# Kernel tuning notes

Measured on AMD Instinct MI355X. Metric: run time of the kernel, lower is better.

The kernel has to match this reference:

```python
import jax, jax.numpy as jnp
import numpy as np

NEG_SLOPE = 0.2

def gat_conv(x, src, dst, W, a_src, a_dst, bias, num_nodes, heads, out_ch, concat):
    # x: [N, Fin]; W: [Fin, heads*out_ch]; a_src/a_dst: [heads, out_ch]
    h = (x @ W).reshape(num_nodes, heads, out_ch)            # [N,H,C]
    alpha_s = jnp.einsum('nhc,hc->nh', h, a_src)             # [N,H]
    alpha_d = jnp.einsum('nhc,hc->nh', h, a_dst)             # [N,H]
    e = alpha_s[src] + alpha_d[dst]                          # [E,H]
    e = jnp.where(e > 0, e, NEG_SLOPE * e)                   # LeakyReLU
    # segment softmax over incoming edges per destination node
    m = jax.ops.segment_max(e, dst, num_segments=num_nodes)  # [N,H]
    m = jnp.where(jnp.isfinite(m), m, 0.0)
    ee = jnp.exp(e - m[dst])                                 # [E,H]
    s = jax.ops.segment_sum(ee, dst, num_segments=num_nodes) # [N,H]
    alpha = ee / (s[dst] + 1e-16)                            # [E,H]
    out = jax.ops.segment_sum(h[src] * alpha[:, :, None], dst,
                              num_segments=num_nodes)        # [N,H,C]
    if concat:
        out = out.reshape(num_nodes, heads * out_ch)
    else:
        out = out.mean(axis=1)
    return out + bias


def setup_inputs() -> dict:
    key = jax.random.key(0)
    ks = jax.random.split(key, 10)
    N, E = 50000, 800000
    EMB, HID, HEADS, REPR = 128, 128, 8, 64
    C1 = HID // HEADS  # 16
    x = jax.random.normal(ks[0], (N, EMB), dtype=jnp.float32)
    edge_index = jax.random.randint(ks[1], (2, E), 0, N, dtype=jnp.int32)
    sc = 1.0 / np.sqrt(EMB)
    W1 = jax.random.normal(ks[2], (EMB, HEADS * C1), dtype=jnp.float32) * sc
    a1_src = jax.random.normal(ks[3], (HEADS, C1), dtype=jnp.float32) * 0.1
    a1_dst = jax.random.normal(ks[4], (HEADS, C1), dtype=jnp.float32) * 0.1
    b1 = jnp.zeros((HID,), dtype=jnp.float32)
    sc2 = 1.0 / np.sqrt(HID)
    W2 = jax.random.normal(ks[5], (HID, REPR), dtype=jnp.float32) * sc2
    a2_src = jax.random.normal(ks[6], (1, REPR), dtype=jnp.float32) * 0.1
    a2_dst = jax.random.normal(ks[7], (1, REPR), dtype=jnp.float32) * 0.1
    b2 = jnp.zeros((REPR,), dtype=jnp.float32)
    return {"x": x, "edge_index": edge_index,
            "W1": W1, "a1_src": a1_src, "a1_dst": a1_dst, "b1": b1,
            "W2": W2, "a2_src": a2_src, "a2_dst": a2_dst, "b2": b2}


def reference(x, edge_index, W1, a1_src, a1_dst, b1, W2, a2_src, a2_dst, b2):
    N = x.shape[0]
    # PyG GATConv adds self-loops by default
    loops = jnp.arange(N, dtype=edge_index.dtype)
    src = jnp.concatenate([edge_index[0], loops])
    dst = jnp.concatenate([edge_index[1], loops])
    # eval mode: F.dropout(p=0.6) is identity
    h = gat_conv(x, src, dst, W1, a1_src, a1_dst, b1, N,
                 heads=8, out_ch=16, concat=True)
    h = jax.nn.elu(h)
    out = gat_conv(h, src, dst, W2, a2_src, a2_dst, b2, N,
                   heads=1, out_ch=64, concat=True)
    return out
```

## Files before the change

kernel.cpp:

```cpp
#include <hip/hip_runtime.h>
#include <hip/hip_fp16.h>
#include <math.h>


typedef _Float16 f16x8 __attribute__((ext_vector_type(8)));
typedef float f32x4 __attribute__((ext_vector_type(4)));

#define PAD 16

__device__ __forceinline__ float leaky_exp(float e) {
    e = (e > 0.f) ? e : 0.2f * e;
    return __expf(e);
}

__device__ __forceinline__ void acc16(float w, float4 hv0, float4 hv1,
                                      float* __restrict__ acc) {
    const __half2* p0 = (const __half2*)&hv0;
    const __half2* p1 = (const __half2*)&hv1;
#pragma unroll
    for (int k = 0; k < 4; k++) {
        float2 f = __half22float2(p0[k]);
        acc[2 * k] += w * f.x;
        acc[2 * k + 1] += w * f.y;
    }
#pragma unroll
    for (int k = 0; k < 4; k++) {
        float2 f = __half22float2(p1[k]);
        acc[8 + 2 * k] += w * f.x;
        acc[8 + 2 * k + 1] += w * f.y;
    }
}

__device__ __forceinline__ void acc8(float w, float4 hv,
                                     float* __restrict__ acc) {
    const __half2* hp = (const __half2*)&hv;
#pragma unroll
    for (int k = 0; k < 4; k++) {
        float2 f = __half22float2(hp[k]);
        acc[2 * k] += w * f.x;
        acc[2 * k + 1] += w * f.y;
    }
}

__global__ __launch_bounds__(256) void augw_hist_kernel(
        const float* __restrict__ W1, const float* __restrict__ a1s,
        const float* __restrict__ a1d, const float* __restrict__ W2,
        const float* __restrict__ a2s, const float* __restrict__ a2d,
        _Float16* __restrict__ W1t, _Float16* __restrict__ W2t,
        const int* __restrict__ dst, int E, int* __restrict__ deg8) {
    int t = threadIdx.x;
    if (blockIdx.x == 0) {
        for (int i = t; i < 144 * 128; i += 256) {
            int c = i >> 7, k = i & 127;
            float v;
            if (c < 128) {
                v = W1[k * 128 + c];
            } else if (c < 136) {
                int h = c - 128; v = 0.f;
#pragma unroll
                for (int j = 0; j < 16; j++) v += W1[k * 128 + h * 16 + j] * a1s[h * 16 + j];
            } else {
                int h = c - 136; v = 0.f;
#pragma unroll
                for (int j = 0; j < 16; j++) v += W1[k * 128 + h * 16 + j] * a1d[h * 16 + j];
            }
            W1t[c * 128 + k] = (_Float16)v;
        }
    } else if (blockIdx.x == 1) {
        for (int i = t; i < 80 * 128; i += 256) {
            int c = i >> 7, k = i & 127;
            float v = 0.f;
            if (c < 64) {
                v = W2[k * 64 + c];
            } else if (c == 64) {
                for (int j = 0; j < 64; j++) v += W2[k * 64 + j] * a2s[j];
            } else if (c == 65) {
                for (int j = 0; j < 64; j++) v += W2[k * 64 + j] * a2d[j];
            }
            W2t[c * 128 + k] = (_Float16)v;
        }
    } else {
        int bid = blockIdx.x - 2;
        int c = bid & 7;
        int i = (bid * 256 + t) * 4;
        if (i + 3 < E) {
            int4 d = *(const int4*)(dst + i);
            atomicAdd(&deg8[d.x * 8 + c], 1);
            atomicAdd(&deg8[d.y * 8 + c], 1);
            atomicAdd(&deg8[d.z * 8 + c], 1);
            atomicAdd(&deg8[d.w * 8 + c], 1);
        } else {
            for (int k = i; k < E; k++) atomicAdd(&deg8[dst[k] * 8 + c], 1);
        }
    }
}

__global__ __launch_bounds__(256) void scan1_kernel(const int* __restrict__ deg8, int N,
                                                    int* __restrict__ rowstart,
                                                    int* __restrict__ blocksum) {
    __shared__ int tmp[256];
    int t = threadIdx.x;
    int i = blockIdx.x * 256 + t;
    int v = 0;
    if (i < N) {
        int4 a = *(const int4*)(deg8 + i * 8);
        int4 b = *(const int4*)(deg8 + i * 8 + 4);
        v = a.x + a.y + a.z + a.w + b.x + b.y + b.z + b.w;
    }
    tmp[t] = v;
    __syncthreads();
    for (int off = 1; off < 256; off <<= 1) {
        int x = (t >= off) ? tmp[t - off] : 0;
        __syncthreads();
        tmp[t] += x;
        __syncthreads();
    }
    if (i < N) rowstart[i] = tmp[t] - v;
    if (t == 255) blocksum[blockIdx.x] = tmp[t];
}

__global__ __launch_bounds__(256) void scan23_kernel(int* __restrict__ rowstart,
                                                     const int* __restrict__ blocksum,
                                                     int nb,
                                                     int* __restrict__ cursor,
                                                     int N, int E) {
    __shared__ int sdata[256];
    int t = threadIdx.x;
    int b = blockIdx.x;
    sdata[t] = (t < nb && t < b) ? blocksum[t] : 0;
    __syncthreads();
#pragma unroll
    for (int off = 128; off > 0; off >>= 1) {
        if (t < off) sdata[t] += sdata[t + off];
        __syncthreads();
    }
    int offset = sdata[0];
    int i = b * 256 + t;
    if (i < N) {
        int v = rowstart[i] + offset;
        rowstart[i] = v;
        cursor[i * PAD] = v;
    } else if (i == N) {
        rowstart[N] = E;
    }
}

__global__ __launch_bounds__(256) void gemm1_scatter_kernel(
        const float* __restrict__ x, const _Float16* __restrict__ W1t,
        __half* __restrict__ h1, float* __restrict__ als,
        float* __restrict__ ald, int N, int gridG1,
        const int* __restrict__ src, const int* __restrict__ dst, int E,
        int* __restrict__ cursor, int* __restrict__ esrc) {
    __shared__ _Float16 Xs[64 * 136];
    int t = threadIdx.x;
    if ((int)blockIdx.x >= gridG1) {
        int sbid = blockIdx.x - gridG1;
        int b = sbid & 7;
        int chunk = sbid >> 3;
        int bdiv = (N + 7) >> 3;
        int blo = b * bdiv;
        int bhi = blo + bdiv;
        int base = chunk * 1024 + t;
#pragma unroll
        for (int u = 0; u < 4; u++) {
            int i = base + u * 256;
            if (i < E) {
                int d = dst[i];
                int s = src[i];
                if (d >= blo && d < bhi) {
                    int p = atomicAdd(&cursor[d * PAD], 1);
                    esrc[p] = s;
                }
            }
        }
        return;
    }
    int row0 = blockIdx.x * 64;
    for (int i = t; i < 2048; i += 256) {
        int r = i >> 5, c4 = i & 31;
        int gr = row0 + r;
        float4 v = make_float4(0.f, 0.f, 0.f, 0.f);
        if (gr < N) v = *(const float4*)(x + (size_t)gr * 128 + c4 * 4);
        _Float16* dp = Xs + r * 136 + c4 * 4;
        dp[0] = (_Float16)v.x; dp[1] = (_Float16)v.y;
        dp[2] = (_Float16)v.z; dp[3] = (_Float16)v.w;
    }
    __syncthreads();
    int w = t >> 6, L = t & 63, m = L & 15, quad = L >> 4;
    f32x4 acc[9];
#pragma unroll
    for (int f = 0; f < 9; f++) acc[f] = (f32x4){0.f, 0.f, 0.f, 0.f};
    const _Float16* Arow = Xs + (w * 16 + m) * 136 + quad * 8;
    const _Float16* Brow = W1t + m * 128 + quad * 8;
#pragma unroll
    for (int kt = 0; kt < 4; kt++) {
        f16x8 a = *(const f16x8*)(Arow + kt * 32);
#pragma unroll
        for (int f = 0; f < 9; f++) {
            f16x8 b = *(const f16x8*)(Brow + f * 2048 + kt * 32);
            acc[f] = __builtin_amdgcn_mfma_f32_16x16x32_f16(a, b, acc[f], 0, 0, 0);
        }
    }
    int nbase = row0 + w * 16 + quad * 4;
#pragma unroll
    for (int r = 0; r < 4; r++) {
        int n = nbase + r;
        if (n < N) {
            __half* hrow = h1 + (size_t)n * 128 + m;
#pragma unroll
            for (int f = 0; f < 8; f++) hrow[f * 16] = __float2half(acc[f][r]);
            float v = acc[8][r];
            if (m < 8) als[n * 8 + m] = v;
            else ald[n * 8 + (m - 8)] = v;
        }
    }
}

__global__ __launch_bounds__(256) void agg1_kernel(const __half* __restrict__ h1,
                                                   const float* __restrict__ als,
                                                   const float* __restrict__ ald,
                                                   const int* __restrict__ rowstart,
                                                   const int* __restrict__ esrc,
                                                   const float* __restrict__ b1,
                                                   __half* __restrict__ act1, int N) {
    int t = threadIdx.x;
    int lane = t & 63;
    int grp = lane >> 3;
    int q = lane & 7;
    int bdiv = (N + 7) >> 3;
    int ln = (blockIdx.x >> 3) * 32 + (t >> 6) * 8 + grp;
    if (ln >= bdiv) return;
    int n = (blockIdx.x & 7) * bdiv + ln;
    if (n >= N) return;
    const float4* h1v = (const float4*)h1;
    float adv = ald[n * 8 + q];
    float acc[16];
#pragma unroll
    for (int k = 0; k < 16; k++) acc[k] = 0.f;
    float wsum = 0.f;
    {
        float w = leaky_exp(als[n * 8 + q] + adv);
        wsum += w;
        acc16(w, h1v[(size_t)n * 16 + 2 * q], h1v[(size_t)n * 16 + 2 * q + 1], acc);
    }
    int beg = rowstart[n], end = rowstart[n + 1];
    int j = beg;
    for (; j + 4 <= end; j += 4) {
        int s0 = esrc[j], s1 = esrc[j + 1], s2 = esrc[j + 2], s3 = esrc[j + 3];
        float4 a0 = h1v[(size_t)s0 * 16 + 2 * q], b0 = h1v[(size_t)s0 * 16 + 2 * q + 1];
        float4 a1 = h1v[(size_t)s1 * 16 + 2 * q], b1 = h1v[(size_t)s1 * 16 + 2 * q + 1];
        float4 a2 = h1v[(size_t)s2 * 16 + 2 * q], b2 = h1v[(size_t)s2 * 16 + 2 * q + 1];
        float4 a3 = h1v[(size_t)s3 * 16 + 2 * q], b3 = h1v[(size_t)s3 * 16 + 2 * q + 1];
        float e0 = als[s0 * 8 + q], e1 = als[s1 * 8 + q];
        float e2 = als[s2 * 8 + q], e3 = als[s3 * 8 + q];
        float w0 = leaky_exp(e0 + adv), w1 = leaky_exp(e1 + adv);
        float w2 = leaky_exp(e2 + adv), w3 = leaky_exp(e3 + adv);
        wsum += (w0 + w1) + (w2 + w3);
        acc16(w0, a0, b0, acc);
        acc16(w1, a1, b1, acc);
        acc16(w2, a2, b2, acc);
        acc16(w3, a3, b3, acc);
    }
    for (; j < end; j++) {
        int s = esrc[j];
        float w = leaky_exp(als[s * 8 + q] + adv);
        wsum += w;
        acc16(w, h1v[(size_t)s * 16 + 2 * q], h1v[(size_t)s * 16 + 2 * q + 1], acc);
    }
    float inv = 1.f / (wsum + 1e-16f);
    const float* bf = b1 + q * 16;
    __align__(16) __half2 po[8];
#pragma unroll
    for (int k = 0; k < 8; k++) {
        float o0 = acc[2 * k] * inv + bf[2 * k];
        float o1 = acc[2 * k + 1] * inv + bf[2 * k + 1];
        o0 = (o0 > 0.f) ? o0 : (__expf(o0) - 1.f);
        o1 = (o1 > 0.f) ? o1 : (__expf(o1) - 1.f);
        po[k] = __floats2half2_rn(o0, o1);
    }
    float4* ov = (float4*)(act1 + (size_t)n * 128 + q * 16);
    ov[0] = ((float4*)po)[0];
    ov[1] = ((float4*)po)[1];
}

__global__ __launch_bounds__(256) void gemm2_kernel(const __half* __restrict__ act1,
                                                    const _Float16* __restrict__ W2t,
                                                    __half* __restrict__ h2,
                                                    float* __restrict__ al2s,
                                                    float* __restrict__ al2d, int N) {
    int t = threadIdx.x;
    int row0 = blockIdx.x * 64;
    int w = t >> 6, L = t & 63, m = L & 15, quad = L >> 4;
    f32x4 acc[5];
#pragma unroll
    for (int f = 0; f < 5; f++) acc[f] = (f32x4){0.f, 0.f, 0.f, 0.f};
    const _Float16* Arow =
        (const _Float16*)act1 + (size_t)(row0 + w * 16 + m) * 128 + quad * 8;
    const _Float16* Brow = W2t + m * 128 + quad * 8;
#pragma unroll
    for (int kt = 0; kt < 4; kt++) {
        f16x8 a = *(const f16x8*)(Arow + kt * 32);
#pragma unroll
        for (int f = 0; f < 5; f++) {
            f16x8 b = *(const f16x8*)(Brow + f * 2048 + kt * 32);
            acc[f] = __builtin_amdgcn_mfma_f32_16x16x32_f16(a, b, acc[f], 0, 0, 0);
        }
    }
    int nbase = row0 + w * 16 + quad * 4;
#pragma unroll
    for (int r = 0; r < 4; r++) {
        int n = nbase + r;
        if (n < N) {
            __half* hrow = h2 + (size_t)n * 64 + m;
#pragma unroll
            for (int f = 0; f < 4; f++) hrow[f * 16] = __float2half(acc[f][r]);
            if (m == 0) al2s[n] = acc[4][r];
            else if (m == 1) al2d[n] = acc[4][r];
        }
    }
}

__global__ __launch_bounds__(256) void agg2_kernel(const __half* __restrict__ h2,
                                                   const float* __restrict__ al2s,
                                                   const float* __restrict__ al2d,
                                                   const int* __restrict__ rowstart,
                                                   const int* __restrict__ esrc,
                                                   const float* __restrict__ b2,
                                                   float* __restrict__ out, int N) {
    int t = threadIdx.x;
    int lane = t & 63;
    int grp = lane >> 3;
    int q = lane & 7;
    int bdiv = (N + 7) >> 3;
    int ln = (blockIdx.x >> 3) * 32 + (t >> 6) * 8 + grp;
    if (ln >= bdiv) return;
    int n = (blockIdx.x & 7) * bdiv + ln;
    if (n >= N) return;
    const float4* h2v = (const float4*)h2;
    float adv = al2d[n];
    float acc[8];
#pragma unroll
    for (int k = 0; k < 8; k++) acc[k] = 0.f;
    float wsum = 0.f;
    {
        float w = leaky_exp(al2s[n] + adv);
        wsum += w;
        acc8(w, h2v[(size_t)n * 8 + q], acc);
    }
    int beg = rowstart[n], end = rowstart[n + 1];
    int j = beg;
    for (; j + 4 <= end; j += 4) {
        int s0 = esrc[j], s1 = esrc[j + 1], s2 = esrc[j + 2], s3 = esrc[j + 3];
        float4 a0 = h2v[(size_t)s0 * 8 + q];
        float4 a1 = h2v[(size_t)s1 * 8 + q];
        float4 a2 = h2v[(size_t)s2 * 8 + q];
        float4 a3 = h2v[(size_t)s3 * 8 + q];
        float e0 = al2s[s0], e1 = al2s[s1], e2 = al2s[s2], e3 = al2s[s3];
        float w0 = leaky_exp(e0 + adv), w1 = leaky_exp(e1 + adv);
        float w2 = leaky_exp(e2 + adv), w3 = leaky_exp(e3 + adv);
        wsum += (w0 + w1) + (w2 + w3);
        acc8(w0, a0, acc);
        acc8(w1, a1, acc);
        acc8(w2, a2, acc);
        acc8(w3, a3, acc);
    }
    for (; j < end; j++) {
        int s = esrc[j];
        float w = leaky_exp(al2s[s] + adv);
        wsum += w;
        acc8(w, h2v[(size_t)s * 8 + q], acc);
    }
    float inv = 1.f / (wsum + 1e-16f);
    const float* bf = b2 + q * 8;
    float4* ov = (float4*)(out + (size_t)n * 64 + q * 8);
    ov[0] = make_float4(acc[0] * inv + bf[0], acc[1] * inv + bf[1],
                        acc[2] * inv + bf[2], acc[3] * inv + bf[3]);
    ov[1] = make_float4(acc[4] * inv + bf[4], acc[5] * inv + bf[5],
                        acc[6] * inv + bf[6], acc[7] * inv + bf[7]);
}

extern "C" void kernel_launch(void* const* d_in, const int* in_sizes, int n_in,
                              void* d_out, int out_size, void* d_ws, size_t ws_size,
                              hipStream_t stream) {
    (void)n_in; (void)out_size; (void)ws_size;
    const float* x   = (const float*)d_in[0];
    const int*   ei  = (const int*)d_in[1];
    const float* W1  = (const float*)d_in[2];
    const float* a1s = (const float*)d_in[3];
    const float* a1d = (const float*)d_in[4];
    const float* b1  = (const float*)d_in[5];
    const float* W2  = (const float*)d_in[6];
    const float* a2s = (const float*)d_in[7];
    const float* a2d = (const float*)d_in[8];
    const float* b2  = (const float*)d_in[9];
    float* out = (float*)d_out;

    const int N = in_sizes[0] / 128;
    const int E = in_sizes[1] / 2;
    const int* src = ei;
    const int* dst = ei + E;

    char* wp = (char*)d_ws;
    auto alloc = [&](size_t bytes) -> void* {
        void* p = (void*)wp;
        wp += (bytes + 255) & ~(size_t)255;
        return p;
    };
    __half* h1   = (__half*)alloc((size_t)N * 128 * 2);
    __half* act1 = (__half*)alloc((size_t)N * 128 * 2);
    __half* h2   = (__half*)alloc((size_t)N * 64 * 2 + 64 * 256);
    float* al1s = (float*)alloc((size_t)N * 8 * 4);
    float* al1d = (float*)alloc((size_t)N * 8 * 4);
    float* al2s = (float*)alloc((size_t)N * 4);
    float* al2d = (float*)alloc((size_t)N * 4);
    int* deg8     = (int*)alloc((size_t)N * 8 * 4);
    int* rowstart = (int*)alloc((size_t)(N + 1) * 4);
    int* cursor   = (int*)alloc((size_t)N * PAD * 4);
    int* esrc     = (int*)alloc((size_t)E * 4);
    int* blocksum = (int*)alloc(256 * 4);
    _Float16* W1t = (_Float16*)alloc(144 * 128 * 2);
    _Float16* W2t = (_Float16*)alloc(80 * 128 * 2);

    const int nbScan = (N + 255) / 256;
    const int gridH  = (E + 1023) / 1024;
    const int gridG1 = (N + 63) / 64;
    const int gridScat = ((E + 1023) / 1024) * 8;
    const int gridG2 = (N + 63) / 64;
    const int bdiv = (N + 7) / 8;
    const int gridAggN = 8 * ((bdiv + 31) / 32);

    hipMemsetAsync(deg8, 0, (size_t)N * 8 * 4, stream);

    augw_hist_kernel<<<2 + gridH, 256, 0, stream>>>(W1, a1s, a1d, W2, a2s, a2d,
                                                    W1t, W2t, dst, E, deg8);
    scan1_kernel<<<nbScan, 256, 0, stream>>>(deg8, N, rowstart, blocksum);
    scan23_kernel<<<(N + 256) / 256, 256, 0, stream>>>(rowstart, blocksum, nbScan,
                                                       cursor, N, E);
    gemm1_scatter_kernel<<<gridG1 + gridScat, 256, 0, stream>>>(
        x, W1t, h1, al1s, al1d, N, gridG1, src, dst, E, cursor, esrc);

    agg1_kernel<<<gridAggN, 256, 0, stream>>>(h1, al1s, al1d, rowstart, esrc, b1, act1, N);
    gemm2_kernel<<<gridG2, 256, 0, stream>>>(act1, W2t, h2, al2s, al2d, N);
    agg2_kernel<<<gridAggN, 256, 0, stream>>>(h2, al2s, al2d, rowstart, esrc, b2, out, N);
}
```

Measured before the change: 261.2 us.

## Pre-bucket edges by destination range in histogram pass to cut scatter reads

The histogram kernel now also partitions (src,dst) pairs into 8 destination-range buckets, using shared-memory local counters and one global atomic per bucket per block. The scatter blocks then read only their own bucket's pairs instead of every block scanning the whole edge list and filtering by destination range. This removes the 8x redundant reads of src/dst in the scatter phase. In exchange it writes an extra pairs buffer of 8 bytes per edge and adds shared and global atomics to the histogram kernel. It also allocates 8*E int2 of workspace, which is a large allocation. The memset is extended to also clear the bucket counters, which relies on bucketCnt being allocated right after deg8 within the 256-byte alignment scheme.

```diff
diff --git a/kernel.cpp b/kernel.cpp
--- a/kernel.cpp
+++ b/kernel.cpp
@@ -47,7 +47,11 @@
         const float* __restrict__ a1d, const float* __restrict__ W2,
         const float* __restrict__ a2s, const float* __restrict__ a2d,
         _Float16* __restrict__ W1t, _Float16* __restrict__ W2t,
-        const int* __restrict__ dst, int E, int* __restrict__ deg8) {
+        const int* __restrict__ src, const int* __restrict__ dst,
+        int E, int N, int* __restrict__ deg8,
+        int* __restrict__ bucketCnt, int2* __restrict__ pairs) {
+    __shared__ int lcnt[8];
+    __shared__ int lbase[8];
     int t = threadIdx.x;
     if (blockIdx.x == 0) {
         for (int i = t; i < 144 * 128; i += 256) {
@@ -66,7 +70,9 @@
             }
             W1t[c * 128 + k] = (_Float16)v;
         }
-    } else if (blockIdx.x == 1) {
+        return;
+    }
+    if (blockIdx.x == 1) {
         for (int i = t; i < 80 * 128; i += 256) {
             int c = i >> 7, k = i & 127;
             float v = 0.f;
@@ -79,19 +85,39 @@
             }
             W2t[c * 128 + k] = (_Float16)v;
         }
+        return;
+    }
+    if (t < 8) lcnt[t] = 0;
+    __syncthreads();
+    int bid = blockIdx.x - 2;
+    int c = bid & 7;
+    int bdiv = (N + 7) >> 3;
+    int i0 = (bid * 256 + t) * 4;
+    int s_[4], d_[4], bk[4], rk[4];
+    int nv = 0;
+    if (i0 + 3 < E) {
+        int4 d4 = *(const int4*)(dst + i0);
+        int4 s4 = *(const int4*)(src + i0);
+        s_[0] = s4.x; s_[1] = s4.y; s_[2] = s4.z; s_[3] = s4.w;
+        d_[0] = d4.x; d_[1] = d4.y; d_[2] = d4.z; d_[3] = d4.w;
+        nv = 4;
     } else {
-        int bid = blockIdx.x - 2;
-        int c = bid & 7;
-        int i = (bid * 256 + t) * 4;
-        if (i + 3 < E) {
-            int4 d = *(const int4*)(dst + i);
-            atomicAdd(&deg8[d.x * 8 + c], 1);
-            atomicAdd(&deg8[d.y * 8 + c], 1);
-            atomicAdd(&deg8[d.z * 8 + c], 1);
-            atomicAdd(&deg8[d.w * 8 + c], 1);
-        } else {
-            for (int k = i; k < E; k++) atomicAdd(&deg8[dst[k] * 8 + c], 1);
-        }
+        for (int k = i0; k < E && nv < 4; k++) {
+            s_[nv] = src[k]; d_[nv] = dst[k]; nv++;
+        }
+    }
+#pragma unroll 4
+    for (int k = 0; k < nv; k++) {
+        atomicAdd(&deg8[d_[k] * 8 + c], 1);
+        bk[k] = d_[k] / bdiv;
+        rk[k] = atomicAdd(&lcnt[bk[k]], 1);
+    }
+    __syncthreads();
+    if (t < 8) lbase[t] = atomicAdd(&bucketCnt[t * 16], lcnt[t]);
+    __syncthreads();
+#pragma unroll 4
+    for (int k = 0; k < nv; k++) {
+        pairs[(size_t)bk[k] * E + lbase[bk[k]] + rk[k]] = make_int2(s_[k], d_[k]);
     }
 }
 
@@ -149,7 +175,8 @@
         const float* __restrict__ x, const _Float16* __restrict__ W1t,
         __half* __restrict__ h1, float* __restrict__ als,
         float* __restrict__ ald, int N, int gridG1,
-        const int* __restrict__ src, const int* __restrict__ dst, int E,
+        const int* __restrict__ bucketCnt, const int2* __restrict__ pairs,
+        int E, int nChunk,
         int* __restrict__ cursor, int* __restrict__ esrc) {
     __shared__ _Float16 Xs[64 * 136];
     int t = threadIdx.x;
@@ -157,19 +184,16 @@
         int sbid = blockIdx.x - gridG1;
         int b = sbid & 7;
         int chunk = sbid >> 3;
-        int bdiv = (N + 7) >> 3;
-        int blo = b * bdiv;
-        int bhi = blo + bdiv;
-        int base = chunk * 1024 + t;
-#pragma unroll
-        for (int u = 0; u < 4; u++) {
-            int i = base + u * 256;
-            if (i < E) {
-                int d = dst[i];
-                int s = src[i];
-                if (d >= blo && d < bhi) {
-                    int p = atomicAdd(&cursor[d * PAD], 1);
-                    esrc[p] = s;
+        int cnt = bucketCnt[b * 16];
+        const int2* plist = pairs + (size_t)b * E;
+        for (int ii = chunk * 1024; ii < cnt; ii += nChunk * 1024) {
+#pragma unroll
+            for (int u = 0; u < 4; u++) {
+                int i = ii + u * 256 + t;
+                if (i < cnt) {
+                    int2 p = plist[i];
+                    int pos = atomicAdd(&cursor[p.y * PAD], 1);
+                    esrc[pos] = p.x;
                 }
             }
         }
@@ -414,9 +438,11 @@
     float* al2s = (float*)alloc((size_t)N * 4);
     float* al2d = (float*)alloc((size_t)N * 4);
     int* deg8     = (int*)alloc((size_t)N * 8 * 4);
+    int* bucketCnt = (int*)alloc(8 * 16 * 4);
     int* rowstart = (int*)alloc((size_t)(N + 1) * 4);
     int* cursor   = (int*)alloc((size_t)N * PAD * 4);
     int* esrc     = (int*)alloc((size_t)E * 4);
+    int2* pairs   = (int2*)alloc((size_t)8 * E * 8);
     int* blocksum = (int*)alloc(256 * 4);
     _Float16* W1t = (_Float16*)alloc(144 * 128 * 2);
     _Float16* W2t = (_Float16*)alloc(80 * 128 * 2);
@@ -424,20 +450,23 @@
     const int nbScan = (N + 255) / 256;
     const int gridH  = (E + 1023) / 1024;
     const int gridG1 = (N + 63) / 64;
-    const int gridScat = ((E + 1023) / 1024) * 8;
     const int gridG2 = (N + 63) / 64;
     const int bdiv = (N + 7) / 8;
     const int gridAggN = 8 * ((bdiv + 31) / 32);
-
-    hipMemsetAsync(deg8, 0, (size_t)N * 8 * 4, stream);
+    const int nChunk = ((E + 7) / 8 + 1023) / 1024 + 2;
+    const int gridScat = 8 * nChunk;
+
+    hipMemsetAsync(deg8, 0, (size_t)N * 8 * 4 + 8 * 16 * 4, stream);
 
     augw_hist_kernel<<<2 + gridH, 256, 0, stream>>>(W1, a1s, a1d, W2, a2s, a2d,
-                                                    W1t, W2t, dst, E, deg8);
+                                                    W1t, W2t, src, dst, E, N,
+                                                    deg8, bucketCnt, pairs);
     scan1_kernel<<<nbScan, 256, 0, stream>>>(deg8, N, rowstart, blocksum);
     scan23_kernel<<<(N + 256) / 256, 256, 0, stream>>>(rowstart, blocksum, nbScan,
                                                        cursor, N, E);
     gemm1_scatter_kernel<<<gridG1 + gridScat, 256, 0, stream>>>(
-        x, W1t, h1, al1s, al1d, N, gridG1, src, dst, E, cursor, esrc);
+        x, W1t, h1, al1s, al1d, N, gridG1, bucketCnt, pairs, E, nChunk,
+        cursor, esrc);
 
     agg1_kernel<<<gridAggN, 256, 0, stream>>>(h1, al1s, al1d, rowstart, esrc, b1, act1, N);
     gemm2_kernel<<<gridG2, 256, 0, stream>>>(act1, W2t, h2, al2s, al2d, N);
```

New measurement: 257.2 us. Within noise of the previous version (-1.5%).
